# Optimization experiments

Measured on AMD Instinct MI355X. Metric: run time of the kernel, lower is better.

Reference implementation:

```python
import jax, jax.numpy as jnp
import numpy as np

D = 1024
N = 64
EPS = 1e-6


def setup_inputs() -> dict:
    key = jax.random.key(0)
    ks = jax.random.split(key, 10)
    sD = 1.0 / np.sqrt(D)
    sN = 1.0 / np.sqrt(N)
    x = jax.random.normal(ks[0], (8, 4096, D), dtype=jnp.float32)
    A_log = jax.random.normal(ks[1], (N,), dtype=jnp.float32)
    WB = jax.random.uniform(ks[2], (N, D), jnp.float32, -sD, sD)
    bB = jax.random.uniform(ks[3], (N,), jnp.float32, -sD, sD)
    WC = jax.random.uniform(ks[4], (N, D), jnp.float32, -sD, sD)
    bC = jax.random.uniform(ks[5], (N,), jnp.float32, -sD, sD)
    Wd = jax.random.uniform(ks[6], (1, D), jnp.float32, -sD, sD)
    bd = jax.random.uniform(ks[7], (1,), jnp.float32, -sD, sD)
    Wo = jax.random.uniform(ks[8], (D, N), jnp.float32, -sN, sN)
    bo = jax.random.uniform(ks[9], (D,), jnp.float32, -sN, sN)
    return {"x": x, "A_log": A_log, "WB": WB, "bB": bB, "WC": WC, "bC": bC,
            "Wd": Wd, "bd": bd, "Wo": Wo, "bo": bo}


def reference(x, A_log, WB, bB, WC, bC, Wd, bd, Wo, bo):
    # x: (B, L, D)
    A = -jax.nn.softplus(A_log)                       # (N,)
    B_t = jnp.einsum('bld,nd->bln', x, WB) + bB       # (B, L, N)
    _C_proj = jnp.einsum('bld,nd->bln', x, WC) + bC   # computed then overwritten in source (dead)
    Delta = jax.nn.softplus(jnp.einsum('bld,nd->bln', x, Wd) + bd)  # (B, L, 1)
    dA = jnp.exp(A * Delta)                           # (B, L, N)
    dB = (dA - 1.0) / (A + EPS) * B_t                 # (B, L, N)
    conv = jnp.cumprod(dA, axis=1)
    ones = jnp.ones_like(dA[:, :1, :])
    Ct = jnp.concatenate([ones, conv[:, :-1, :]], axis=1)  # shifted cumprod (replaces C_t)
    z = dB / (Ct + EPS)
    s = jnp.cumsum(z, axis=1)
    X_state = Ct * s                                  # x_init = 0
    Y = jnp.einsum('bln,dn->bld', Ct * X_state, Wo) + bo
    return Y
```

## Files before the change

kernel.cpp:

```cpp
#include <hip/hip_runtime.h>
#include <math.h>

#define DDIM 1024
#define NCH 64
#define LSEQ 4096
#define NBATCH 8
#define NROWS (NBATCH * LSEQ)
#define EPSF 1e-6f
#define NCK 64
#define CLEN 64

__device__ __forceinline__ float softplusf(float v) {
    return (v > 20.0f) ? v : log1pf(expf(v));
}

__global__ void prep_kernel(const float* __restrict__ Wo, float* __restrict__ WoT) {
    int id = blockIdx.x * 256 + threadIdx.x;
    int n = id >> 10;
    int d = id & (DDIM - 1);
    WoT[n * DDIM + d] = Wo[d * NCH + n];
}

#define MT 128
#define KSPL 2
#define KRNG (DDIM / KSPL)
#define SUBK 32

__global__ __launch_bounds__(256, 2) void proj2_kernel(
        const float* __restrict__ x,
        const float* __restrict__ WB,
        const float* __restrict__ Wd,
        float* __restrict__ Bt0, float* __restrict__ Bt1,
        float* __restrict__ De0, float* __restrict__ De1) {
    __shared__ float x_lds[MT][36];
    const int t  = threadIdx.x;
    const int tr = t & 31;
    const int tc = t >> 5;
    const int rt = blockIdx.x >> 1;
    const int ks = blockIdx.x & 1;
    const int R0 = rt * MT;
    const int kb0 = ks * KRNG;

    float acc[4][8];
    #pragma unroll
    for (int i = 0; i < 4; i++)
        #pragma unroll
        for (int j = 0; j < 8; j++) acc[i][j] = 0.0f;
    float dpart = 0.0f;

    for (int kk = 0; kk < KRNG; kk += SUBK) {
        const int kb = kb0 + kk;
        __syncthreads();
        #pragma unroll
        for (int p = 0; p < 4; p++) {
            const int row = p * 32 + (t >> 3);
            const int c   = (t & 7) * 4;
            const float4 v = *reinterpret_cast<const float4*>(
                &x[(size_t)(R0 + row) * DDIM + kb + c]);
            *reinterpret_cast<float4*>(&x_lds[row][c]) = v;
        }
        __syncthreads();

        if (t < MT) {
            #pragma unroll 8
            for (int k = 0; k < SUBK; k++)
                dpart = fmaf(x_lds[t][k], Wd[kb + k], dpart);
        }

        #pragma unroll
        for (int k4 = 0; k4 < SUBK / 4; k4++) {
            float4 wv[8];
            #pragma unroll
            for (int j = 0; j < 8; j++)
                wv[j] = *reinterpret_cast<const float4*>(
                    &WB[(size_t)(tc * 8 + j) * DDIM + kb + k4 * 4]);
            float4 xv[4];
            #pragma unroll
            for (int i = 0; i < 4; i++)
                xv[i] = *reinterpret_cast<const float4*>(&x_lds[tr + 32 * i][k4 * 4]);
            #pragma unroll
            for (int i = 0; i < 4; i++)
                #pragma unroll
                for (int j = 0; j < 8; j++) {
                    acc[i][j] = fmaf(xv[i].x, wv[j].x, acc[i][j]);
                    acc[i][j] = fmaf(xv[i].y, wv[j].y, acc[i][j]);
                    acc[i][j] = fmaf(xv[i].z, wv[j].z, acc[i][j]);
                    acc[i][j] = fmaf(xv[i].w, wv[j].w, acc[i][j]);
                }
        }
    }

    float* Bt = ks ? Bt1 : Bt0;
    #pragma unroll
    for (int i = 0; i < 4; i++) {
        const size_t base = (size_t)(R0 + tr + 32 * i) * NCH + tc * 8;
        *reinterpret_cast<float4*>(&Bt[base])     = make_float4(acc[i][0], acc[i][1], acc[i][2], acc[i][3]);
        *reinterpret_cast<float4*>(&Bt[base + 4]) = make_float4(acc[i][4], acc[i][5], acc[i][6], acc[i][7]);
    }
    if (t < MT) (ks ? De1 : De0)[R0 + t] = dpart;
}

__global__ __launch_bounds__(256) void gate_kernel(
        const float* __restrict__ A_log, const float* __restrict__ bB,
        const float* __restrict__ bd,
        const float* __restrict__ De0, const float* __restrict__ De1,
        float* __restrict__ dA_g,
        float* __restrict__ dBG) {
    const int t   = threadIdx.x;
    const int n   = t & 63;
    const int row = blockIdx.x * 4 + (t >> 6);
    const size_t idx = (size_t)row * NCH + n;
    const float a   = -softplusf(A_log[n]);
    const float dlt = softplusf(De0[row] + De1[row] + bd[0]);
    const float Btv = dBG[idx] + dA_g[idx] + bB[n];
    const float dAv = expf(a * dlt);
    const float dBv = (dAv - 1.0f) / (a + EPSF) * Btv;
    dA_g[idx] = dAv;
    dBG[idx]  = dBv;
}

__global__ __launch_bounds__(64) void chunkprod_kernel(
        const float* __restrict__ dA_g, float* __restrict__ P) {
    const int n = threadIdx.x;
    const int blk = blockIdx.x;
    size_t base = (size_t)blk * CLEN * NCH + n;
    float p = 1.0f;
    #pragma unroll 8
    for (int u = 0; u < CLEN; u++) p *= dA_g[base + (size_t)u * NCH];
    P[(size_t)blk * NCH + n] = p;
}

__global__ __launch_bounds__(512) void stitch1_kernel(
        const float* __restrict__ P, float* __restrict__ E) {
    const int id = threadIdx.x;
    const int b = id >> 6, n = id & 63;
    size_t idx = (size_t)b * NCK * NCH + n;
    float e = 1.0f;
    for (int j0 = 0; j0 < NCK; j0 += 8) {
        float p8[8];
        #pragma unroll
        for (int u = 0; u < 8; u++) p8[u] = P[idx + (size_t)(j0 + u) * NCH];
        #pragma unroll
        for (int u = 0; u < 8; u++) {
            E[idx + (size_t)(j0 + u) * NCH] = e;
            e *= p8[u];
        }
    }
}

__global__ __launch_bounds__(64) void chunkz_kernel(
        const float* __restrict__ dA_g, const float* __restrict__ dB_g,
        const float* __restrict__ E, float* __restrict__ Z) {
    const int n = threadIdx.x;
    const int blk = blockIdx.x;
    size_t base = (size_t)blk * CLEN * NCH + n;
    const float e = E[(size_t)blk * NCH + n];
    float L = 1.0f, zs = 0.0f;
    #pragma unroll 8
    for (int u = 0; u < CLEN; u++) {
        const float a  = dA_g[base + (size_t)u * NCH];
        const float bv = dB_g[base + (size_t)u * NCH];
        const float c  = e * L;
        zs += bv / (c + EPSF);
        L *= a;
    }
    Z[(size_t)blk * NCH + n] = zs;
}

__global__ __launch_bounds__(512) void stitch2_kernel(
        const float* __restrict__ Z, float* __restrict__ S) {
    const int id = threadIdx.x;
    const int b = id >> 6, n = id & 63;
    size_t idx = (size_t)b * NCK * NCH + n;
    float s = 0.0f;
    for (int j0 = 0; j0 < NCK; j0 += 8) {
        float z8[8];
        #pragma unroll
        for (int u = 0; u < 8; u++) z8[u] = Z[idx + (size_t)(j0 + u) * NCH];
        #pragma unroll
        for (int u = 0; u < 8; u++) {
            S[idx + (size_t)(j0 + u) * NCH] = s;
            s += z8[u];
        }
    }
}

__global__ __launch_bounds__(64) void chunkout_kernel(
        const float* __restrict__ dA_g, float* __restrict__ dBG,
        const float* __restrict__ E, const float* __restrict__ S) {
    const int n = threadIdx.x;
    const int blk = blockIdx.x;
    size_t base = (size_t)blk * CLEN * NCH + n;
    const float e = E[(size_t)blk * NCH + n];
    float L = 1.0f;
    float s = S[(size_t)blk * NCH + n];
    #pragma unroll 8
    for (int u = 0; u < CLEN; u++) {
        const float a  = dA_g[base + (size_t)u * NCH];
        const float bv = dBG [base + (size_t)u * NCH];
        const float c  = e * L;
        s += bv / (c + EPSF);
        dBG[base + (size_t)u * NCH] = c * c * s;
        L *= a;
    }
}

__global__ __launch_bounds__(256, 4) void out2_kernel(
        const float* __restrict__ G,
        const float* __restrict__ WoT,
        const float* __restrict__ bo,
        float* __restrict__ Y) {
    __shared__ float g_lds[NCH][36];
    const int t  = threadIdx.x;
    const int tc = t & 63;
    const int tr = t >> 6;
    const int R0 = (blockIdx.x >> 1) * 32;
    const int D0 = (blockIdx.x & 1) * 512;

    {
        const int grow = t >> 3;
        const int gn0  = (t & 7) * 8;
        const float4 a0 = *reinterpret_cast<const float4*>(&G[(size_t)(R0 + grow) * NCH + gn0]);
        const float4 a1 = *reinterpret_cast<const float4*>(&G[(size_t)(R0 + grow) * NCH + gn0 + 4]);
        g_lds[gn0 + 0][grow] = a0.x; g_lds[gn0 + 1][grow] = a0.y;
        g_lds[gn0 + 2][grow] = a0.z; g_lds[gn0 + 3][grow] = a0.w;
        g_lds[gn0 + 4][grow] = a1.x; g_lds[gn0 + 5][grow] = a1.y;
        g_lds[gn0 + 6][grow] = a1.z; g_lds[gn0 + 7][grow] = a1.w;
    }
    __syncthreads();

    float acc[8][8];
    #pragma unroll
    for (int i = 0; i < 8; i++)
        #pragma unroll
        for (int j = 0; j < 8; j++) acc[i][j] = 0.0f;

    const size_t wcol = (size_t)D0 + tc * 8;
    for (int n = 0; n < NCH; n++) {
        const float4 g0 = *reinterpret_cast<const float4*>(&g_lds[n][tr * 8]);
        const float4 g1 = *reinterpret_cast<const float4*>(&g_lds[n][tr * 8 + 4]);
        const float4 w0 = *reinterpret_cast<const float4*>(&WoT[(size_t)n * DDIM + wcol]);
        const float4 w1 = *reinterpret_cast<const float4*>(&WoT[(size_t)n * DDIM + wcol + 4]);
        const float ga[8] = {g0.x, g0.y, g0.z, g0.w, g1.x, g1.y, g1.z, g1.w};
        const float wa[8] = {w0.x, w0.y, w0.z, w0.w, w1.x, w1.y, w1.z, w1.w};
        #pragma unroll
        for (int i = 0; i < 8; i++)
            #pragma unroll
            for (int j = 0; j < 8; j++)
                acc[i][j] = fmaf(ga[i], wa[j], acc[i][j]);
    }

    const float4 b0 = *reinterpret_cast<const float4*>(&bo[wcol]);
    const float4 b1 = *reinterpret_cast<const float4*>(&bo[wcol + 4]);
    #pragma unroll
    for (int i = 0; i < 8; i++) {
        const size_t yb = (size_t)(R0 + tr * 8 + i) * DDIM + wcol;
        *reinterpret_cast<float4*>(&Y[yb]) =
            make_float4(acc[i][0] + b0.x, acc[i][1] + b0.y, acc[i][2] + b0.z, acc[i][3] + b0.w);
        *reinterpret_cast<float4*>(&Y[yb + 4]) =
            make_float4(acc[i][4] + b1.x, acc[i][5] + b1.y, acc[i][6] + b1.z, acc[i][7] + b1.w);
    }
}

extern "C" void kernel_launch(void* const* d_in, const int* in_sizes, int n_in,
                              void* d_out, int out_size, void* d_ws, size_t ws_size,
                              hipStream_t stream) {
    const float* x     = (const float*)d_in[0];
    const float* A_log = (const float*)d_in[1];
    const float* WB    = (const float*)d_in[2];
    const float* bB    = (const float*)d_in[3];
    const float* Wd    = (const float*)d_in[6];
    const float* bd    = (const float*)d_in[7];
    const float* Wo    = (const float*)d_in[8];
    const float* bo    = (const float*)d_in[9];
    float* Y = (float*)d_out;

    float* dA_g = (float*)d_ws;
    float* dBG  = dA_g + (size_t)NROWS * NCH;
    float* WoT  = dBG  + (size_t)NROWS * NCH;
    float* P    = WoT  + (size_t)NCH * DDIM;
    float* E    = P    + (size_t)NBATCH * NCK * NCH;
    float* Z    = E    + (size_t)NBATCH * NCK * NCH;
    float* S    = Z    + (size_t)NBATCH * NCK * NCH;
    float* De0  = S    + (size_t)NBATCH * NCK * NCH;
    float* De1  = De0  + (size_t)NROWS;

    const int NCHUNKS = NBATCH * NCK;

    prep_kernel<<<dim3(256), dim3(256), 0, stream>>>(Wo, WoT);
    proj2_kernel<<<dim3((NROWS / MT) * KSPL), dim3(256), 0, stream>>>(
        x, WB, Wd, dBG, dA_g, De0, De1);
    gate_kernel<<<dim3(NROWS / 4), dim3(256), 0, stream>>>(
        A_log, bB, bd, De0, De1, dA_g, dBG);
    chunkprod_kernel<<<dim3(NCHUNKS), dim3(64), 0, stream>>>(dA_g, P);
    stitch1_kernel<<<dim3(1), dim3(512), 0, stream>>>(P, E);
    chunkz_kernel<<<dim3(NCHUNKS), dim3(64), 0, stream>>>(dA_g, dBG, E, Z);
    stitch2_kernel<<<dim3(1), dim3(512), 0, stream>>>(Z, S);
    chunkout_kernel<<<dim3(NCHUNKS), dim3(64), 0, stream>>>(dA_g, dBG, E, S);
    out2_kernel<<<dim3((NROWS / 32) * 2), dim3(256), 0, stream>>>(dBG, WoT, bo, Y);
}
```

Before: 409.3 us.

## Split projection K four ways and shorten scan chunks for more parallelism

The projection GEMM now splits the reduction dimension across four blocks instead of two, writing four partial buffers that the gate kernel sums. The chunked scan uses 256 chunks of length 16 instead of 64 of 64, so the chunk kernels launch four times as many blocks. The stitch kernels now run one block per batch. This raises occupancy in the latency-bound scan and projection stages, at the cost of extra partial-sum memory traffic and longer serial stitch loops.

```diff
diff --git a/kernel.cpp b/kernel.cpp
--- a/kernel.cpp
+++ b/kernel.cpp
@@ -7,8 +7,10 @@
 #define NBATCH 8
 #define NROWS (NBATCH * LSEQ)
 #define EPSF 1e-6f
-#define NCK 64
-#define CLEN 64
+#define NCK 256
+#define CLEN 16
+#define NM ((size_t)NROWS * NCH)
+#define SC ((size_t)NBATCH * NCK * NCH)
 
 __device__ __forceinline__ float softplusf(float v) {
     return (v > 20.0f) ? v : log1pf(expf(v));
@@ -22,22 +24,22 @@
 }
 
 #define MT 128
-#define KSPL 2
+#define KSPL 4
 #define KRNG (DDIM / KSPL)
 #define SUBK 32
 
-__global__ __launch_bounds__(256, 2) void proj2_kernel(
+__global__ __launch_bounds__(256, 4) void proj2_kernel(
         const float* __restrict__ x,
         const float* __restrict__ WB,
         const float* __restrict__ Wd,
-        float* __restrict__ Bt0, float* __restrict__ Bt1,
-        float* __restrict__ De0, float* __restrict__ De1) {
+        float* __restrict__ Part,
+        float* __restrict__ DeAll) {
     __shared__ float x_lds[MT][36];
     const int t  = threadIdx.x;
     const int tr = t & 31;
     const int tc = t >> 5;
-    const int rt = blockIdx.x >> 1;
-    const int ks = blockIdx.x & 1;
+    const int rt = blockIdx.x >> 2;
+    const int ks = blockIdx.x & 3;
     const int R0 = rt * MT;
     const int kb0 = ks * KRNG;
 
@@ -90,33 +92,34 @@
         }
     }
 
-    float* Bt = ks ? Bt1 : Bt0;
+    float* Bt = Part + (size_t)ks * NM;
     #pragma unroll
     for (int i = 0; i < 4; i++) {
         const size_t base = (size_t)(R0 + tr + 32 * i) * NCH + tc * 8;
         *reinterpret_cast<float4*>(&Bt[base])     = make_float4(acc[i][0], acc[i][1], acc[i][2], acc[i][3]);
         *reinterpret_cast<float4*>(&Bt[base + 4]) = make_float4(acc[i][4], acc[i][5], acc[i][6], acc[i][7]);
     }
-    if (t < MT) (ks ? De1 : De0)[R0 + t] = dpart;
+    if (t < MT) DeAll[(size_t)ks * NROWS + R0 + t] = dpart;
 }
 
 __global__ __launch_bounds__(256) void gate_kernel(
         const float* __restrict__ A_log, const float* __restrict__ bB,
         const float* __restrict__ bd,
-        const float* __restrict__ De0, const float* __restrict__ De1,
-        float* __restrict__ dA_g,
-        float* __restrict__ dBG) {
+        const float* __restrict__ DeAll,
+        float* __restrict__ Part) {
     const int t   = threadIdx.x;
     const int n   = t & 63;
     const int row = blockIdx.x * 4 + (t >> 6);
     const size_t idx = (size_t)row * NCH + n;
     const float a   = -softplusf(A_log[n]);
-    const float dlt = softplusf(De0[row] + De1[row] + bd[0]);
-    const float Btv = dBG[idx] + dA_g[idx] + bB[n];
+    const float dsum = DeAll[row] + DeAll[NROWS + row]
+                     + DeAll[2 * (size_t)NROWS + row] + DeAll[3 * (size_t)NROWS + row];
+    const float dlt = softplusf(dsum + bd[0]);
+    const float Btv = Part[idx] + Part[idx + NM] + Part[idx + 2 * NM] + Part[idx + 3 * NM] + bB[n];
     const float dAv = expf(a * dlt);
     const float dBv = (dAv - 1.0f) / (a + EPSF) * Btv;
-    dA_g[idx] = dAv;
-    dBG[idx]  = dBv;
+    Part[idx + NM] = dAv;
+    Part[idx]      = dBv;
 }
 
 __global__ __launch_bounds__(64) void chunkprod_kernel(
@@ -125,25 +128,24 @@
     const int blk = blockIdx.x;
     size_t base = (size_t)blk * CLEN * NCH + n;
     float p = 1.0f;
-    #pragma unroll 8
+    #pragma unroll
     for (int u = 0; u < CLEN; u++) p *= dA_g[base + (size_t)u * NCH];
     P[(size_t)blk * NCH + n] = p;
 }
 
-__global__ __launch_bounds__(512) void stitch1_kernel(
+__global__ __launch_bounds__(64) void stitch1_kernel(
         const float* __restrict__ P, float* __restrict__ E) {
-    const int id = threadIdx.x;
-    const int b = id >> 6, n = id & 63;
+    const int b = blockIdx.x, n = threadIdx.x;
     size_t idx = (size_t)b * NCK * NCH + n;
     float e = 1.0f;
-    for (int j0 = 0; j0 < NCK; j0 += 8) {
-        float p8[8];
-        #pragma unroll
-        for (int u = 0; u < 8; u++) p8[u] = P[idx + (size_t)(j0 + u) * NCH];
-        #pragma unroll
-        for (int u = 0; u < 8; u++) {
+    for (int j0 = 0; j0 < NCK; j0 += 16) {
+        float p16[16];
+        #pragma unroll
+        for (int u = 0; u < 16; u++) p16[u] = P[idx + (size_t)(j0 + u) * NCH];
+        #pragma unroll
+        for (int u = 0; u < 16; u++) {
             E[idx + (size_t)(j0 + u) * NCH] = e;
-            e *= p8[u];
+            e *= p16[u];
         }
     }
 }
@@ -156,7 +158,7 @@
     size_t base = (size_t)blk * CLEN * NCH + n;
     const float e = E[(size_t)blk * NCH + n];
     float L = 1.0f, zs = 0.0f;
-    #pragma unroll 8
+    #pragma unroll
     for (int u = 0; u < CLEN; u++) {
         const float a  = dA_g[base + (size_t)u * NCH];
         const float bv = dB_g[base + (size_t)u * NCH];
@@ -167,20 +169,19 @@
     Z[(size_t)blk * NCH + n] = zs;
 }
 
-__global__ __launch_bounds__(512) void stitch2_kernel(
+__global__ __launch_bounds__(64) void stitch2_kernel(
         const float* __restrict__ Z, float* __restrict__ S) {
-    const int id = threadIdx.x;
-    const int b = id >> 6, n = id & 63;
+    const int b = blockIdx.x, n = threadIdx.x;
     size_t idx = (size_t)b * NCK * NCH + n;
     float s = 0.0f;
-    for (int j0 = 0; j0 < NCK; j0 += 8) {
-        float z8[8];
-        #pragma unroll
-        for (int u = 0; u < 8; u++) z8[u] = Z[idx + (size_t)(j0 + u) * NCH];
-        #pragma unroll
-        for (int u = 0; u < 8; u++) {
+    for (int j0 = 0; j0 < NCK; j0 += 16) {
+        float z16[16];
+        #pragma unroll
+        for (int u = 0; u < 16; u++) z16[u] = Z[idx + (size_t)(j0 + u) * NCH];
+        #pragma unroll
+        for (int u = 0; u < 16; u++) {
             S[idx + (size_t)(j0 + u) * NCH] = s;
-            s += z8[u];
+            s += z16[u];
         }
     }
 }
@@ -194,7 +195,7 @@
     const float e = E[(size_t)blk * NCH + n];
     float L = 1.0f;
     float s = S[(size_t)blk * NCH + n];
-    #pragma unroll 8
+    #pragma unroll
     for (int u = 0; u < CLEN; u++) {
         const float a  = dA_g[base + (size_t)u * NCH];
         const float bv = dBG [base + (size_t)u * NCH];
@@ -275,27 +276,27 @@
     const float* bo    = (const float*)d_in[9];
     float* Y = (float*)d_out;
 
-    float* dA_g = (float*)d_ws;
-    float* dBG  = dA_g + (size_t)NROWS * NCH;
-    float* WoT  = dBG  + (size_t)NROWS * NCH;
-    float* P    = WoT  + (size_t)NCH * DDIM;
-    float* E    = P    + (size_t)NBATCH * NCK * NCH;
-    float* Z    = E    + (size_t)NBATCH * NCK * NCH;
-    float* S    = Z    + (size_t)NBATCH * NCK * NCH;
-    float* De0  = S    + (size_t)NBATCH * NCK * NCH;
-    float* De1  = De0  + (size_t)NROWS;
+    float* Part = (float*)d_ws;
+    float* dBG  = Part;
+    float* dA_g = Part + NM;
+    float* WoT  = Part + 4 * NM;
+    float* P    = WoT + (size_t)NCH * DDIM;
+    float* E    = P + SC;
+    float* Z    = E + SC;
+    float* S    = Z + SC;
+    float* DeAll = S + SC;
 
     const int NCHUNKS = NBATCH * NCK;
 
     prep_kernel<<<dim3(256), dim3(256), 0, stream>>>(Wo, WoT);
     proj2_kernel<<<dim3((NROWS / MT) * KSPL), dim3(256), 0, stream>>>(
-        x, WB, Wd, dBG, dA_g, De0, De1);
+        x, WB, Wd, Part, DeAll);
     gate_kernel<<<dim3(NROWS / 4), dim3(256), 0, stream>>>(
-        A_log, bB, bd, De0, De1, dA_g, dBG);
+        A_log, bB, bd, DeAll, Part);
     chunkprod_kernel<<<dim3(NCHUNKS), dim3(64), 0, stream>>>(dA_g, P);
-    stitch1_kernel<<<dim3(1), dim3(512), 0, stream>>>(P, E);
+    stitch1_kernel<<<dim3(NBATCH), dim3(64), 0, stream>>>(P, E);
     chunkz_kernel<<<dim3(NCHUNKS), dim3(64), 0, stream>>>(dA_g, dBG, E, Z);
-    stitch2_kernel<<<dim3(1), dim3(512), 0, stream>>>(Z, S);
+    stitch2_kernel<<<dim3(NBATCH), dim3(64), 0, stream>>>(Z, S);
     chunkout_kernel<<<dim3(NCHUNKS), dim3(64), 0, stream>>>(dA_g, dBG, E, S);
     out2_kernel<<<dim3((NROWS / 32) * 2), dim3(256), 0, stream>>>(dBG, WoT, bo, Y);
 }
```

Measured after the change: 470.0 us. 1.15x slower.
